# Performance work log

Hardware: AMD Instinct MI355X
Metric: run time of the kernel (lower is better)

## Reference

```python
import jax, jax.numpy as jnp
import numpy as np

FEATURE_DIM = 256


def setup_inputs() -> dict:
    key = jax.random.key(0)
    ks = jax.random.split(key, 8)
    B, C, H, W = 4, FEATURE_DIM, 64, 64
    s = 1.0 / np.sqrt(C)
    return {
        "x1": jax.random.normal(ks[0], (B, C, H, W), dtype=jnp.float32),
        "x2": jax.random.normal(ks[1], (B, C, H, W), dtype=jnp.float32),
        "Wq": jax.random.uniform(ks[2], (C, C), jnp.float32, -s, s),
        "bq": jax.random.uniform(ks[3], (C,), jnp.float32, -s, s),
        "Wk": jax.random.uniform(ks[4], (C, C), jnp.float32, -s, s),
        "bk": jax.random.uniform(ks[5], (C,), jnp.float32, -s, s),
        "Wv": jax.random.uniform(ks[6], (C, C), jnp.float32, -s, s),
        "bv": jax.random.uniform(ks[7], (C,), jnp.float32, -s, s),
    }


def _linear(x, W, b):
    # torch nn.Linear: x @ W.T + b
    return jnp.einsum("bnc,dc->bnd", x, W) + b


def reference(x1, x2, Wq, bq, Wk, bk, Wv, bv):
    B, C, H, W = x1.shape
    # flatten spatial -> tokens: [B, N, C]
    t1 = x1.reshape(B, C, H * W).transpose(0, 2, 1)
    t2 = x2.reshape(B, C, H * W).transpose(0, 2, 1)

    q1, k1, v1 = _linear(t1, Wq, bq), _linear(t1, Wk, bk), _linear(t1, Wv, bv)
    q2, k2, v2 = _linear(t2, Wq, bq), _linear(t2, Wk, bk), _linear(t2, Wv, bv)

    # NOTE: original module has NO 1/sqrt(d) scaling, and attends to v of the
    # SAME stream as the query (x1_out uses v1, x2_out uses v2) — keep faithful.
    a1 = jax.nn.softmax(jnp.einsum("bnc,bmc->bnm", q1, k2), axis=-1)
    a2 = jax.nn.softmax(jnp.einsum("bnc,bmc->bnm", q2, k1), axis=-1)

    o1 = jnp.einsum("bnm,bmc->bnc", a1, v1)
    o2 = jnp.einsum("bnm,bmc->bnc", a2, v2)

    x1_out = o1.transpose(0, 2, 1).reshape(B, C, H, W)
    x2_out = o2.transpose(0, 2, 1).reshape(B, C, H, W)
    return (x1_out, x2_out)
```

## Files before the change

### kernel.cpp

```cpp
#include <hip/hip_runtime.h>
#include <hip/hip_bf16.h>
#include <string.h>

typedef _Float16 half8 __attribute__((ext_vector_type(8)));
typedef _Float16 half4 __attribute__((ext_vector_type(4)));
typedef float f32x4 __attribute__((ext_vector_type(4)));
typedef float f32x16 __attribute__((ext_vector_type(16)));

#define NTOK 4096
#define CDIM 256

#define GLD_LDS16(g, l) __builtin_amdgcn_global_load_lds( \
    (const __attribute__((address_space(1))) void*)(g), \
    (__attribute__((address_space(3))) void*)(l), 16, 0, 0)

static __device__ __forceinline__ unsigned pk16(float a, float b) {
    auto h = __builtin_amdgcn_cvt_pkrtz(a, b);
    unsigned u;
    __builtin_memcpy(&u, &h, 4);
    return u;
}

__global__ __launch_bounds__(256, 2) void proj_kernel(
    const float* __restrict__ x1, const float* __restrict__ x2,
    const float* __restrict__ Wq, const float* __restrict__ bq,
    const float* __restrict__ Wk, const float* __restrict__ bk,
    const float* __restrict__ Wv, const float* __restrict__ bv,
    _Float16* __restrict__ Qh, _Float16* __restrict__ Kh,
    _Float16* __restrict__ Vt)
{
    __shared__ __align__(16) _Float16 Xl[64][264];
    __shared__ __align__(16) _Float16 Wl[64][264];
    __shared__ __align__(16) _Float16 Ol[64][68];

    const int t = threadIdx.x;
    const int lane = t & 63;
    const int w = t >> 6;
    const int bs = blockIdx.x >> 6;
    const int ntile = blockIdx.x & 63;
    const int n0 = ntile * 64;
    const int s = bs & 1, b = bs >> 1;

    const float* x = (s ? x2 : x1) + (size_t)b * CDIM * NTOK;

#pragma unroll
    for (int i = 0; i < 16; i++) {
        int id = t + 256 * i;
        int c = id >> 4, n4 = (id & 15) * 4;
        float4 v = *(const float4*)(x + (size_t)c * NTOK + n0 + n4);
        Xl[n4 + 0][c] = (_Float16)v.x;
        Xl[n4 + 1][c] = (_Float16)v.y;
        Xl[n4 + 2][c] = (_Float16)v.z;
        Xl[n4 + 3][c] = (_Float16)v.w;
    }

    for (int proj = 0; proj < 3; proj++) {
        const float* Wp = proj == 0 ? Wq : (proj == 1 ? Wk : Wv);
        const float* bp = proj == 0 ? bq : (proj == 1 ? bk : bv);
        for (int dt = 0; dt < 4; dt++) {
            const int d0 = dt * 64;
            __syncthreads();
#pragma unroll
            for (int i = 0; i < 16; i++) {
                int id = t + 256 * i;
                int d = id >> 6, c4 = (id & 63) * 4;
                float4 v = *(const float4*)(Wp + (size_t)(d0 + d) * CDIM + c4);
                half4 h = { (_Float16)v.x, (_Float16)v.y, (_Float16)v.z, (_Float16)v.w };
                *(half4*)&Wl[d][c4] = h;
            }
            __syncthreads();

            f32x4 acc[4];
            const f32x4 fz = {0.f, 0.f, 0.f, 0.f};
#pragma unroll
            for (int nt = 0; nt < 4; nt++) acc[nt] = fz;
#pragma unroll
            for (int cc = 0; cc < 8; cc++) {
                half8 wf = *(const half8*)&Wl[16 * w + (lane & 15)][cc * 32 + (lane >> 4) * 8];
#pragma unroll
                for (int nt = 0; nt < 4; nt++) {
                    half8 xf = *(const half8*)&Xl[nt * 16 + (lane & 15)][cc * 32 + (lane >> 4) * 8];
                    acc[nt] = __builtin_amdgcn_mfma_f32_16x16x32_f16(wf, xf, acc[nt], 0, 0, 0);
                }
            }
#pragma unroll
            for (int r = 0; r < 4; r++) {
                float bias = bp[d0 + 16 * w + (lane >> 4) * 4 + r];
#pragma unroll
                for (int nt = 0; nt < 4; nt++) {
                    _Float16 hv = (_Float16)(acc[nt][r] + bias);
                    if (proj < 2) Ol[nt * 16 + (lane & 15)][16 * w + (lane >> 4) * 4 + r] = hv;
                    else          Ol[16 * w + (lane >> 4) * 4 + r][nt * 16 + (lane & 15)] = hv;
                }
            }
            __syncthreads();
            _Float16* dst;
            size_t stride;
            if (proj == 0)      { dst = Qh + ((size_t)bs * NTOK + n0) * CDIM + d0; stride = CDIM; }
            else if (proj == 1) { dst = Kh + ((size_t)bs * NTOK + n0) * CDIM + d0; stride = CDIM; }
            else                { dst = Vt + ((size_t)bs * CDIM + d0) * NTOK + n0; stride = NTOK; }
#pragma unroll
            for (int i = 0; i < 4; i++) {
                int id = t + 256 * i;
                int row = id >> 4, c4 = (id & 15) * 4;
                *(half4*)(dst + (size_t)row * stride + c4) = *(const half4*)&Ol[row][c4];
            }
        }
    }
}

__global__ __launch_bounds__(512, 2) void flash_kernel(
    const _Float16* __restrict__ Qh, const _Float16* __restrict__ Kh,
    const _Float16* __restrict__ Vt, float* __restrict__ out)
{
    __shared__ __align__(16) char smem[131072];

    const int t = threadIdx.x, lane = t & 63;
    const int w = t >> 6;
    const int qg = w >> 1, mg = w & 1;
    const int l5 = lane & 31, hi = lane >> 5;
    const int bs = blockIdx.x & 7;
    const int qt = blockIdx.x >> 3;
    const int n0 = qt * 128;
    const int s = bs & 1, b = bs >> 1;

    half8 qf[16];
    {
        const _Float16* qp = Qh + ((size_t)bs * NTOK + n0 + qg * 32 + l5) * CDIM + hi * 8;
#pragma unroll
        for (int cc = 0; cc < 16; cc++) qf[cc] = *(const half8*)(qp + cc * 16);
    }

    const int bsK = b * 2 + (s ^ 1);
    const uint4* const Ksrc = (const uint4*)(Kh + (size_t)bsK * NTOK * CDIM);
    const uint4* const Vsrc = (const uint4*)(Vt + (size_t)bs * CDIM * NTOK);

    float m_run = -1e30f, l_run = 0.f;
    f32x16 Oacc[8];
    const f32x16 FZ16 = {0,0,0,0,0,0,0,0,0,0,0,0,0,0,0,0};
#pragma unroll
    for (int ct = 0; ct < 8; ct++) Oacc[ct] = FZ16;

    auto stage = [&](int buf, int kt) {
        const int m0 = kt * 64;
        char* base = smem + buf * 65536;
        if (w < 4) {
#pragma unroll
            for (int i = 0; i < 8; i++) {
                int instr = w * 8 + i;
                int cc = instr >> 1, mt = instr & 1;
                GLD_LDS16(Ksrc + (size_t)(m0 + mt * 32 + l5) * 32 + cc * 2 + hi,
                          base + (instr * 64) * 16 + (hi * 32 + l5) * 16);
            }
        } else {
#pragma unroll
            for (int i = 0; i < 8; i++) {
                int instr = (w - 4) * 8 + i;
                int kcg = instr >> 3, ct = instr & 7;
                GLD_LDS16(Vsrc + (size_t)(ct * 32 + l5) * 512 + (m0 >> 3) + kcg * 2 + hi,
                          base + 32768 + (instr * 64) * 16 + (hi * 32 + l5) * 16);
            }
        }
    };

    stage(0, 0);
    __syncthreads();

    for (int kt = 0; kt < 64; kt++) {
        const int cur = kt & 1;
        if (kt < 63) stage(cur ^ 1, kt + 1);
        const char* Kb = smem + cur * 65536;
        const char* Vbuf = Kb + 32768;

        f32x16 sf = FZ16;
#pragma unroll
        for (int cc = 0; cc < 16; cc++) {
            half8 kf = *(const half8*)(Kb + (cc * 2 + mg) * 1024 + hi * 512 + l5 * 16);
            sf = __builtin_amdgcn_mfma_f32_32x32x16_f16(kf, qf[cc], sf, 0, 0, 0);
        }

        float pm = sf[0];
#pragma unroll
        for (int r = 1; r < 16; r++) pm = fmaxf(pm, sf[r]);
        pm = fmaxf(pm, __shfl_xor(pm, 32));

        if (__any(pm > m_run + 8.0f)) {
            float nm = fmaxf(m_run, pm);
            float sc = __expf(m_run - nm);
            m_run = nm;
            l_run *= sc;
#pragma unroll
            for (int reg = 0; reg < 16; reg++) {
                float sr = __shfl(sc, (reg & 3) + 8 * (reg >> 2) + 4 * hi);
#pragma unroll
                for (int ct = 0; ct < 8; ct++) Oacc[ct][reg] *= sr;
            }
        }

        float lsum = 0.f;
#pragma unroll
        for (int r = 0; r < 16; r++) {
            float p = __expf(sf[r] - m_run);
            sf[r] = p;
            lsum += p;
        }
        lsum += __shfl_xor(lsum, 32);
        l_run += lsum;

        uint4 paw[2];
#pragma unroll
        for (int kc = 0; kc < 2; kc++) {
            const int qe = kc * 8;
            unsigned A01 = pk16(sf[qe + 0], sf[qe + 1]);
            unsigned A23 = pk16(sf[qe + 2], sf[qe + 3]);
            unsigned B01 = pk16(sf[qe + 4], sf[qe + 5]);
            unsigned B23 = pk16(sf[qe + 6], sf[qe + 7]);
            unsigned d0 = A01, s0 = B01;
            asm volatile("v_permlane32_swap_b32 %0, %1" : "+v"(d0), "+v"(s0));
            unsigned d1 = A23, s1 = B23;
            asm volatile("v_permlane32_swap_b32 %0, %1" : "+v"(d1), "+v"(s1));
            paw[kc].x = d0; paw[kc].y = d1; paw[kc].z = s0; paw[kc].w = s1;
        }

#pragma unroll
        for (int kc = 0; kc < 2; kc++) {
            half8 pa;
            __builtin_memcpy(&pa, &paw[kc], 16);
            const int kcg = mg * 2 + kc;
#pragma unroll
            for (int ct = 0; ct < 8; ct++) {
                half8 vf = *(const half8*)(Vbuf + ((kcg * 8 + ct) * 64) * 16
                                                 + (hi * 32 + l5) * 16);
                Oacc[ct] = __builtin_amdgcn_mfma_f32_32x32x16_f16(pa, vf, Oacc[ct], 0, 0, 0);
            }
        }

        __syncthreads();
    }

    float* const mlbuf = (float*)(smem + 65536);

    if (mg == 1 && hi == 0) {
        *(float2*)(mlbuf + (qg * 32 + l5) * 2) = make_float2(m_run, l_run);
    }
    if (mg == 1) {
#pragma unroll
        for (int ct = 0; ct < 4; ct++)
#pragma unroll
            for (int rc = 0; rc < 4; rc++) {
                f32x4 v = { Oacc[ct][rc*4+0], Oacc[ct][rc*4+1], Oacc[ct][rc*4+2], Oacc[ct][rc*4+3] };
                *(f32x4*)(smem + ((qg * 4 + ct) * 4 + rc) * 1024 + lane * 16) = v;
            }
    }
    __syncthreads();

    float a_s = 0.f, b_s = 0.f;
    if (mg == 0) {
        float2 ml = *(const float2*)(mlbuf + (qg * 32 + l5) * 2);
        float mstar = fmaxf(m_run, ml.x);
        float e0 = __expf(m_run - mstar), e1 = __expf(ml.x - mstar);
        float ltot = l_run * e0 + ml.y * e1;
        a_s = e0 / ltot; b_s = e1 / ltot;
#pragma unroll
        for (int ct = 0; ct < 4; ct++)
#pragma unroll
            for (int rc = 0; rc < 4; rc++) {
                f32x4 o1 = *(const f32x4*)(smem + ((qg * 4 + ct) * 4 + rc) * 1024 + lane * 16);
#pragma unroll
                for (int j = 0; j < 4; j++) {
                    int r = j + 8 * rc + 4 * hi;
                    Oacc[ct][rc*4+j] = Oacc[ct][rc*4+j] * __shfl(a_s, r) + o1[j] * __shfl(b_s, r);
                }
            }
    }
    __syncthreads();
    if (mg == 1) {
#pragma unroll
        for (int ct = 0; ct < 4; ct++)
#pragma unroll
            for (int rc = 0; rc < 4; rc++) {
                f32x4 v = { Oacc[ct+4][rc*4+0], Oacc[ct+4][rc*4+1], Oacc[ct+4][rc*4+2], Oacc[ct+4][rc*4+3] };
                *(f32x4*)(smem + ((qg * 4 + ct) * 4 + rc) * 1024 + lane * 16) = v;
            }
    }
    __syncthreads();
    if (mg == 0) {
#pragma unroll
        for (int ct = 0; ct < 4; ct++)
#pragma unroll
            for (int rc = 0; rc < 4; rc++) {
                f32x4 o1 = *(const f32x4*)(smem + ((qg * 4 + ct) * 4 + rc) * 1024 + lane * 16);
#pragma unroll
                for (int j = 0; j < 4; j++) {
                    int r = j + 8 * rc + 4 * hi;
                    Oacc[ct+4][rc*4+j] = Oacc[ct+4][rc*4+j] * __shfl(a_s, r) + o1[j] * __shfl(b_s, r);
                }
            }
    }

    float* obase = out + (size_t)(s * 4 + b) * CDIM * NTOK + n0;
    char* const Olp = smem;
#pragma unroll
    for (int h = 0; h < 2; h++) {
        __syncthreads();
        if (mg == 0) {
#pragma unroll
            for (int ct4 = 0; ct4 < 4; ct4++) {
                int ct = h * 4 + ct4;
                int cl = ct4 * 32 + l5;
#pragma unroll
                for (int reg = 0; reg < 16; reg++) {
                    int n = qg * 32 + (reg & 3) + 8 * (reg >> 2) + 4 * hi;
                    int byteoff = cl * 512 + n * 4;
                    *(float*)(Olp + (byteoff ^ ((cl & 7) << 4))) = Oacc[ct][reg];
                }
            }
        }
        __syncthreads();
#pragma unroll
        for (int i = 0; i < 8; i++) {
            int id = t + 512 * i;
            int c = id >> 5, nc = id & 31;
            f32x4 v = *(const f32x4*)(Olp + c * 512 + ((nc ^ (c & 7)) << 4));
            *(f32x4*)(obase + (size_t)(h * 128 + c) * NTOK + nc * 4) = v;
        }
    }
}

extern "C" void kernel_launch(void* const* d_in, const int* in_sizes, int n_in,
                              void* d_out, int out_size, void* d_ws, size_t ws_size,
                              hipStream_t stream) {
    const float* x1 = (const float*)d_in[0];
    const float* x2 = (const float*)d_in[1];
    const float* Wq = (const float*)d_in[2];
    const float* bq = (const float*)d_in[3];
    const float* Wk = (const float*)d_in[4];
    const float* bk = (const float*)d_in[5];
    const float* Wv = (const float*)d_in[6];
    const float* bv = (const float*)d_in[7];

    _Float16* Qh = (_Float16*)d_ws;
    _Float16* Kh = Qh + (size_t)8 * NTOK * CDIM;
    _Float16* Vt = Kh + (size_t)8 * NTOK * CDIM;

    proj_kernel<<<dim3(512), dim3(256), 0, stream>>>(x1, x2, Wq, bq, Wk, bk, Wv, bv, Qh, Kh, Vt);
    flash_kernel<<<dim3(256), dim3(512), 0, stream>>>(Qh, Kh, Vt, (float*)d_out);
}
```

Before: 308.0 us.

## Split attention over key halves with separate merge kernel and prescaled exp2 softmax

Adds a new path that pre-converts weights (folding log2e into Wq and bq) and inputs to fp16. It then runs projection from fp16 buffers and a 256-thread flash kernel that splits the key range into two halves across 512 blocks, writing fp16 partial outputs plus running max and sum. A merge kernel combines the two halves. This replaces the intra-block split-K reduction with a grid-level one and uses exp2 instead of expf. The cost is extra launches, an fp16 rounding of partial outputs, and extra global traffic for the partial results, and the path runs only when the workspace is large enough.

```diff
diff --git a/kernel.cpp b/kernel.cpp
--- a/kernel.cpp
+++ b/kernel.cpp
@@ -9,6 +9,7 @@
 
 #define NTOK 4096
 #define CDIM 256
+#define LOG2E 1.44269504f
 
 #define GLD_LDS16(g, l) __builtin_amdgcn_global_load_lds( \
     (const __attribute__((address_space(1))) void*)(g), \
@@ -19,6 +20,343 @@
     unsigned u;
     __builtin_memcpy(&u, &h, 4);
     return u;
+}
+
+
+__global__ __launch_bounds__(256) void cvtW_kernel(
+    const float* __restrict__ Wq, const float* __restrict__ Wk,
+    const float* __restrict__ Wv, _Float16* __restrict__ Wh)
+{
+    int pid = blockIdx.x * 256 + threadIdx.x;
+    int base = pid * 8;
+    int proj = base >> 16;
+    int within = base & 65535;
+    const float* src = (proj == 0 ? Wq : (proj == 1 ? Wk : Wv)) + within;
+    float sc = (proj == 0) ? LOG2E : 1.0f;
+    float4 a = *(const float4*)(src);
+    float4 b = *(const float4*)(src + 4);
+    half8 h = { (_Float16)(a.x*sc), (_Float16)(a.y*sc), (_Float16)(a.z*sc), (_Float16)(a.w*sc),
+                (_Float16)(b.x*sc), (_Float16)(b.y*sc), (_Float16)(b.z*sc), (_Float16)(b.w*sc) };
+    *(half8*)(Wh + base) = h;
+}
+
+__global__ __launch_bounds__(256) void cvtX_kernel(
+    const float* __restrict__ x1, const float* __restrict__ x2,
+    _Float16* __restrict__ Xt)
+{
+    __shared__ __align__(16) _Float16 Xl[64][264];
+    const int t = threadIdx.x;
+    const int bs = blockIdx.x >> 6;
+    const int n0 = (blockIdx.x & 63) * 64;
+    const int s = bs & 1, b = bs >> 1;
+    const float* x = (s ? x2 : x1) + (size_t)b * CDIM * NTOK;
+#pragma unroll
+    for (int i = 0; i < 16; i++) {
+        int id = t + 256 * i;
+        int c = id >> 4, n4 = (id & 15) * 4;
+        float4 v = *(const float4*)(x + (size_t)c * NTOK + n0 + n4);
+        Xl[n4 + 0][c] = (_Float16)v.x;
+        Xl[n4 + 1][c] = (_Float16)v.y;
+        Xl[n4 + 2][c] = (_Float16)v.z;
+        Xl[n4 + 3][c] = (_Float16)v.w;
+    }
+    __syncthreads();
+    uint4* dst = (uint4*)(Xt + ((size_t)bs * NTOK + n0) * CDIM);
+#pragma unroll
+    for (int i = 0; i < 8; i++) {
+        int id = t + 256 * i;
+        int row = id >> 5, ck = id & 31;
+        dst[(size_t)row * 32 + ck] = *(const uint4*)&Xl[row][ck * 8];
+    }
+}
+
+__global__ __launch_bounds__(256, 2) void proj2_kernel(
+    const _Float16* __restrict__ Xt, const _Float16* __restrict__ Wh,
+    const float* __restrict__ bq, const float* __restrict__ bk,
+    const float* __restrict__ bv,
+    _Float16* __restrict__ Qh, _Float16* __restrict__ Kh,
+    _Float16* __restrict__ Vt)
+{
+    __shared__ __align__(16) _Float16 Xl[64][264];
+    __shared__ __align__(16) _Float16 Wl[64][264];
+    __shared__ __align__(16) _Float16 Ol[64][68];
+
+    const int t = threadIdx.x;
+    const int lane = t & 63;
+    const int w = t >> 6;
+    const int bs = blockIdx.x >> 6;
+    const int n0 = (blockIdx.x & 63) * 64;
+
+    const uint4* xsrc = (const uint4*)(Xt + ((size_t)bs * NTOK + n0) * CDIM);
+#pragma unroll
+    for (int i = 0; i < 8; i++) {
+        int id = t + 256 * i;
+        int row = id >> 5, ck = id & 31;
+        *(uint4*)&Xl[row][ck * 8] = xsrc[(size_t)row * 32 + ck];
+    }
+
+    for (int proj = 0; proj < 3; proj++) {
+        const float* bp = proj == 0 ? bq : (proj == 1 ? bk : bv);
+        const float bscale = (proj == 0) ? LOG2E : 1.0f;
+        for (int dt = 0; dt < 4; dt++) {
+            const int d0 = dt * 64;
+            __syncthreads();
+            const uint4* wsrc = (const uint4*)(Wh + ((size_t)proj * 256 + d0) * CDIM);
+#pragma unroll
+            for (int i = 0; i < 8; i++) {
+                int id = t + 256 * i;
+                int row = id >> 5, ck = id & 31;
+                *(uint4*)&Wl[row][ck * 8] = wsrc[(size_t)row * 32 + ck];
+            }
+            __syncthreads();
+
+            f32x4 acc[4];
+            const f32x4 fz = {0.f, 0.f, 0.f, 0.f};
+#pragma unroll
+            for (int nt = 0; nt < 4; nt++) acc[nt] = fz;
+#pragma unroll
+            for (int cc = 0; cc < 8; cc++) {
+                half8 wf = *(const half8*)&Wl[16 * w + (lane & 15)][cc * 32 + (lane >> 4) * 8];
+#pragma unroll
+                for (int nt = 0; nt < 4; nt++) {
+                    half8 xf = *(const half8*)&Xl[nt * 16 + (lane & 15)][cc * 32 + (lane >> 4) * 8];
+                    acc[nt] = __builtin_amdgcn_mfma_f32_16x16x32_f16(wf, xf, acc[nt], 0, 0, 0);
+                }
+            }
+#pragma unroll
+            for (int r = 0; r < 4; r++) {
+                float bias = bp[d0 + 16 * w + (lane >> 4) * 4 + r] * bscale;
+#pragma unroll
+                for (int nt = 0; nt < 4; nt++) {
+                    _Float16 hv = (_Float16)(acc[nt][r] + bias);
+                    if (proj < 2) Ol[nt * 16 + (lane & 15)][16 * w + (lane >> 4) * 4 + r] = hv;
+                    else          Ol[16 * w + (lane >> 4) * 4 + r][nt * 16 + (lane & 15)] = hv;
+                }
+            }
+            __syncthreads();
+            _Float16* dst;
+            size_t stride;
+            if (proj == 0)      { dst = Qh + ((size_t)bs * NTOK + n0) * CDIM + d0; stride = CDIM; }
+            else if (proj == 1) { dst = Kh + ((size_t)bs * NTOK + n0) * CDIM + d0; stride = CDIM; }
+            else                { dst = Vt + ((size_t)bs * CDIM + d0) * NTOK + n0; stride = NTOK; }
+#pragma unroll
+            for (int i = 0; i < 4; i++) {
+                int id = t + 256 * i;
+                int row = id >> 4, c4 = (id & 15) * 4;
+                *(half4*)(dst + (size_t)row * stride + c4) = *(const half4*)&Ol[row][c4];
+            }
+        }
+    }
+}
+
+__global__ __launch_bounds__(256, 2) void flash_half(
+    const _Float16* __restrict__ Qh, const _Float16* __restrict__ Kh,
+    const _Float16* __restrict__ Vt, _Float16* __restrict__ Op,
+    float* __restrict__ Ml)
+{
+    __shared__ __align__(16) char smem[65536];
+
+    const int t = threadIdx.x, lane = t & 63;
+    const int w = t >> 6;
+    const int l5 = lane & 31, hi = lane >> 5;
+    const int bid = blockIdx.x;
+    const int bs = bid & 7;
+    const int rest = bid >> 3;
+    const int qt = rest & 31;
+    const int h = rest >> 5;
+    const int n0 = qt * 128;
+    const int s = bs & 1, b = bs >> 1;
+    const int tokbase = h * 2048;
+
+    half8 qf[16];
+    {
+        const _Float16* qp = Qh + ((size_t)bs * NTOK + n0 + w * 32 + l5) * CDIM + hi * 8;
+#pragma unroll
+        for (int cc = 0; cc < 16; cc++) qf[cc] = *(const half8*)(qp + cc * 16);
+    }
+
+    const int bsK = b * 2 + (s ^ 1);
+    const uint4* const Ku = (const uint4*)(Kh + (size_t)bsK * NTOK * CDIM);
+    const uint4* const Vu = (const uint4*)(Vt + (size_t)bs * CDIM * NTOK);
+
+    float m_run = -1e30f, l_run = 0.f;
+    f32x16 Oacc[8];
+    const f32x16 FZ16 = {0,0,0,0,0,0,0,0,0,0,0,0,0,0,0,0};
+#pragma unroll
+    for (int ct = 0; ct < 8; ct++) Oacc[ct] = FZ16;
+
+    auto stage = [&](int buf, int kt) {
+        const int m0 = tokbase + kt * 32;
+        char* base = smem + buf * 32768;
+#pragma unroll
+        for (int i = 0; i < 4; i++) {
+            int cc = w * 4 + i;
+            GLD_LDS16(Ku + (size_t)(m0 + l5) * 32 + cc * 2 + hi,
+                      base + cc * 1024 + lane * 16);
+        }
+#pragma unroll
+        for (int i = 0; i < 4; i++) {
+            int f = w * 4 + i;
+            int kc = f >> 3, ct = f & 7;
+            GLD_LDS16(Vu + (size_t)(ct * 32 + l5) * 512 + (m0 >> 3) + kc * 2 + hi,
+                      base + 16384 + f * 1024 + lane * 16);
+        }
+    };
+
+    stage(0, 0);
+    __syncthreads();
+
+    for (int kt = 0; kt < 64; kt++) {
+        const int cur = kt & 1;
+        if (kt < 63) stage(cur ^ 1, kt + 1);
+        const char* Kb = smem + cur * 32768;
+        const char* Vb = Kb + 16384;
+
+        f32x16 sfA = FZ16, sfB = FZ16;
+        __builtin_amdgcn_s_setprio(1);
+#pragma unroll
+        for (int cc = 0; cc < 8; cc++) {
+            half8 kfA = *(const half8*)(Kb + cc * 1024 + lane * 16);
+            half8 kfB = *(const half8*)(Kb + (cc + 8) * 1024 + lane * 16);
+            sfA = __builtin_amdgcn_mfma_f32_32x32x16_f16(kfA, qf[cc], sfA, 0, 0, 0);
+            sfB = __builtin_amdgcn_mfma_f32_32x32x16_f16(kfB, qf[cc + 8], sfB, 0, 0, 0);
+        }
+        __builtin_amdgcn_s_setprio(0);
+        f32x16 sf = sfA + sfB;
+
+        float pm = fmaxf(fmaxf(fmaxf(sf[0], sf[1]), fmaxf(sf[2], sf[3])),
+                         fmaxf(fmaxf(sf[4], sf[5]), fmaxf(sf[6], sf[7])));
+        float pm2 = fmaxf(fmaxf(fmaxf(sf[8], sf[9]), fmaxf(sf[10], sf[11])),
+                          fmaxf(fmaxf(sf[12], sf[13]), fmaxf(sf[14], sf[15])));
+        pm = fmaxf(pm, pm2);
+        pm = fmaxf(pm, __shfl_xor(pm, 32));
+
+        if (__any(pm > m_run + 11.54f)) {
+            float nm = fmaxf(m_run, pm);
+            float sc = exp2f(m_run - nm);
+            m_run = nm;
+            l_run *= sc;
+#pragma unroll
+            for (int reg = 0; reg < 16; reg++) {
+                float sr = __shfl(sc, (reg & 3) + 8 * (reg >> 2) + 4 * hi);
+#pragma unroll
+                for (int ct = 0; ct < 8; ct++) Oacc[ct][reg] *= sr;
+            }
+        }
+
+#pragma unroll
+        for (int r = 0; r < 16; r++) sf[r] = exp2f(sf[r] - m_run);
+
+        uint4 paw[2];
+#pragma unroll
+        for (int kc = 0; kc < 2; kc++) {
+            const int qe = kc * 8;
+            unsigned A01 = pk16(sf[qe + 0], sf[qe + 1]);
+            unsigned A23 = pk16(sf[qe + 2], sf[qe + 3]);
+            unsigned B01 = pk16(sf[qe + 4], sf[qe + 5]);
+            unsigned B23 = pk16(sf[qe + 6], sf[qe + 7]);
+            unsigned d0 = A01, s0 = B01;
+            asm volatile("v_permlane32_swap_b32 %0, %1" : "+v"(d0), "+v"(s0));
+            unsigned d1 = A23, s1 = B23;
+            asm volatile("v_permlane32_swap_b32 %0, %1" : "+v"(d1), "+v"(s1));
+            paw[kc].x = d0; paw[kc].y = d1; paw[kc].z = s0; paw[kc].w = s1;
+        }
+
+        __builtin_amdgcn_s_setprio(1);
+#pragma unroll
+        for (int kc = 0; kc < 2; kc++) {
+            half8 pa;
+            __builtin_memcpy(&pa, &paw[kc], 16);
+#pragma unroll
+            for (int ct = 0; ct < 8; ct++) {
+                half8 vf = *(const half8*)(Vb + (kc * 8 + ct) * 1024 + lane * 16);
+                Oacc[ct] = __builtin_amdgcn_mfma_f32_32x32x16_f16(pa, vf, Oacc[ct], 0, 0, 0);
+            }
+        }
+        __builtin_amdgcn_s_setprio(0);
+
+        float lsum = ((sf[0] + sf[1]) + (sf[2] + sf[3])) + ((sf[4] + sf[5]) + (sf[6] + sf[7]))
+                   + ((sf[8] + sf[9]) + (sf[10] + sf[11])) + ((sf[12] + sf[13]) + (sf[14] + sf[15]));
+        lsum += __shfl_xor(lsum, 32);
+        l_run += lsum;
+
+        __syncthreads();
+    }
+
+    if (hi == 0) {
+        float2 ml = make_float2(m_run, l_run);
+        *(float2*)(Ml + ((size_t)(h * 8 + bs) * NTOK + n0 + w * 32 + l5) * 2) = ml;
+    }
+
+    _Float16* const Olp = (_Float16*)smem;
+#pragma unroll
+    for (int hcc = 0; hcc < 2; hcc++) {
+        __syncthreads();
+#pragma unroll
+        for (int ct4 = 0; ct4 < 4; ct4++) {
+            int ct = hcc * 4 + ct4;
+            int cl = ct4 * 32 + l5;
+#pragma unroll
+            for (int reg = 0; reg < 16; reg++) {
+                int n = w * 32 + (reg & 3) + 8 * (reg >> 2) + 4 * hi;
+                Olp[cl * 136 + n] = (_Float16)Oacc[ct][reg];
+            }
+        }
+        __syncthreads();
+        _Float16* obase = Op + ((size_t)(h * 8 + bs) * CDIM + hcc * 128) * NTOK + n0;
+#pragma unroll
+        for (int i = 0; i < 8; i++) {
+            int id = t + 256 * i;
+            int c = id >> 4, ch = id & 15;
+            *(uint4*)(obase + (size_t)c * NTOK + ch * 8) = *(const uint4*)&Olp[c * 136 + ch * 8];
+        }
+    }
+}
+
+__global__ __launch_bounds__(256) void merge_kernel(
+    const _Float16* __restrict__ Op, const float* __restrict__ Ml,
+    float* __restrict__ out)
+{
+    __shared__ float w0s[256], w1s[256];
+    const int t = threadIdx.x;
+    const int bid = blockIdx.x;
+    const int bs = bid & 7;
+    const int cb = (bid >> 3) & 7;
+    const int nb = bid >> 6;
+    const int s = bs & 1, b = bs >> 1;
+
+    {
+        int n = nb * 256 + t;
+        float2 ml0 = *(const float2*)(Ml + ((size_t)(0 + bs) * NTOK + n) * 2);
+        float2 ml1 = *(const float2*)(Ml + ((size_t)(8 + bs) * NTOK + n) * 2);
+        float mstar = fmaxf(ml0.x, ml1.x);
+        float e0 = exp2f(ml0.x - mstar), e1 = exp2f(ml1.x - mstar);
+        float inv = 1.0f / (e0 * ml0.y + e1 * ml1.y);
+        w0s[t] = e0 * inv;
+        w1s[t] = e1 * inv;
+    }
+    __syncthreads();
+
+    const size_t cbase0 = ((size_t)(0 + bs) * CDIM + cb * 32) * NTOK + nb * 256;
+    const size_t cbase1 = ((size_t)(8 + bs) * CDIM + cb * 32) * NTOK + nb * 256;
+    float* obase = out + ((size_t)(s * 4 + b) * CDIM + cb * 32) * NTOK + nb * 256;
+#pragma unroll
+    for (int i = 0; i < 4; i++) {
+        int id = t + 256 * i;
+        int c = id >> 5, nc = (id & 31) * 8;
+        half8 a = *(const half8*)(Op + cbase0 + (size_t)c * NTOK + nc);
+        half8 d = *(const half8*)(Op + cbase1 + (size_t)c * NTOK + nc);
+        float4 o0, o1;
+        float* op = &o0.x;
+#pragma unroll
+        for (int j = 0; j < 8; j++) {
+            float v = w0s[nc + j] * (float)a[j] + w1s[nc + j] * (float)d[j];
+            if (j < 4) (&o0.x)[j] = v; else (&o1.x)[j - 4] = v;
+        }
+        (void)op;
+        *(float4*)(obase + (size_t)c * NTOK + nc) = o0;
+        *(float4*)(obase + (size_t)c * NTOK + nc + 4) = o1;
+    }
 }
 
 __global__ __launch_bounds__(256, 2) void proj_kernel(
@@ -37,10 +375,8 @@
     const int lane = t & 63;
     const int w = t >> 6;
     const int bs = blockIdx.x >> 6;
-    const int ntile = blockIdx.x & 63;
-    const int n0 = ntile * 64;
+    const int n0 = (blockIdx.x & 63) * 64;
     const int s = bs & 1, b = bs >> 1;
-
     const float* x = (s ? x2 : x1) + (size_t)b * CDIM * NTOK;
 
 #pragma unroll
@@ -53,7 +389,6 @@
         Xl[n4 + 2][c] = (_Float16)v.z;
         Xl[n4 + 3][c] = (_Float16)v.w;
     }
-
     for (int proj = 0; proj < 3; proj++) {
         const float* Wp = proj == 0 ? Wq : (proj == 1 ? Wk : Wv);
         const float* bp = proj == 0 ? bq : (proj == 1 ? bk : bv);
@@ -65,11 +400,10 @@
                 int id = t + 256 * i;
                 int d = id >> 6, c4 = (id & 63) * 4;
                 float4 v = *(const float4*)(Wp + (size_t)(d0 + d) * CDIM + c4);
-                half4 h = { (_Float16)v.x, (_Float16)v.y, (_Float16)v.z, (_Float16)v.w };
-                *(half4*)&Wl[d][c4] = h;
+                half4 hh = { (_Float16)v.x, (_Float16)v.y, (_Float16)v.z, (_Float16)v.w };
+                *(half4*)&Wl[d][c4] = hh;
             }
             __syncthreads();
-
             f32x4 acc[4];
             const f32x4 fz = {0.f, 0.f, 0.f, 0.f};
 #pragma unroll
@@ -114,7 +448,6 @@
     const _Float16* __restrict__ Vt, float* __restrict__ out)
 {
     __shared__ __align__(16) char smem[131072];
-
     const int t = threadIdx.x, lane = t & 63;
     const int w = t >> 6;
     const int qg = w >> 1, mg = w & 1;
@@ -130,7 +463,6 @@
 #pragma unroll
         for (int cc = 0; cc < 16; cc++) qf[cc] = *(const half8*)(qp + cc * 16);
     }
-
     const int bsK = b * 2 + (s ^ 1);
     const uint4* const Ksrc = (const uint4*)(Kh + (size_t)bsK * NTOK * CDIM);
     const uint4* const Vsrc = (const uint4*)(Vt + (size_t)bs * CDIM * NTOK);
@@ -178,12 +510,10 @@
             half8 kf = *(const half8*)(Kb + (cc * 2 + mg) * 1024 + hi * 512 + l5 * 16);
             sf = __builtin_amdgcn_mfma_f32_32x32x16_f16(kf, qf[cc], sf, 0, 0, 0);
         }
-
         float pm = sf[0];
 #pragma unroll
         for (int r = 1; r < 16; r++) pm = fmaxf(pm, sf[r]);
         pm = fmaxf(pm, __shfl_xor(pm, 32));
-
         if (__any(pm > m_run + 8.0f)) {
             float nm = fmaxf(m_run, pm);
             float sc = __expf(m_run - nm);
@@ -196,7 +526,6 @@
                 for (int ct = 0; ct < 8; ct++) Oacc[ct][reg] *= sr;
             }
         }
-
         float lsum = 0.f;
 #pragma unroll
         for (int r = 0; r < 16; r++) {
@@ -221,7 +550,6 @@
             asm volatile("v_permlane32_swap_b32 %0, %1" : "+v"(d1), "+v"(s1));
             paw[kc].x = d0; paw[kc].y = d1; paw[kc].z = s0; paw[kc].w = s1;
         }
-
 #pragma unroll
         for (int kc = 0; kc < 2; kc++) {
             half8 pa;
@@ -229,17 +557,14 @@
             const int kcg = mg * 2 + kc;
 #pragma unroll
             for (int ct = 0; ct < 8; ct++) {
-                half8 vf = *(const half8*)(Vbuf + ((kcg * 8 + ct) * 64) * 16
-                                                 + (hi * 32 + l5) * 16);
+                half8 vf = *(const half8*)(Vbuf + ((kcg * 8 + ct) * 64) * 16 + (hi * 32 + l5) * 16);
                 Oacc[ct] = __builtin_amdgcn_mfma_f32_32x32x16_f16(pa, vf, Oacc[ct], 0, 0, 0);
             }
         }
-
         __syncthreads();
     }
 
     float* const mlbuf = (float*)(smem + 65536);
-
     if (mg == 1 && hi == 0) {
         *(float2*)(mlbuf + (qg * 32 + l5) * 2) = make_float2(m_run, l_run);
     }
@@ -253,7 +578,6 @@
             }
     }
     __syncthreads();
-
     float a_s = 0.f, b_s = 0.f;
     if (mg == 0) {
         float2 ml = *(const float2*)(mlbuf + (qg * 32 + l5) * 2);
@@ -297,16 +621,15 @@
                 }
             }
     }
-
     float* obase = out + (size_t)(s * 4 + b) * CDIM * NTOK + n0;
     char* const Olp = smem;
 #pragma unroll
-    for (int h = 0; h < 2; h++) {
+    for (int hh = 0; hh < 2; hh++) {
         __syncthreads();
         if (mg == 0) {
 #pragma unroll
             for (int ct4 = 0; ct4 < 4; ct4++) {
-                int ct = h * 4 + ct4;
+                int ct = hh * 4 + ct4;
                 int cl = ct4 * 32 + l5;
 #pragma unroll
                 for (int reg = 0; reg < 16; reg++) {
@@ -322,7 +645,7 @@
             int id = t + 512 * i;
             int c = id >> 5, nc = id & 31;
             f32x4 v = *(const f32x4*)(Olp + c * 512 + ((nc ^ (c & 7)) << 4));
-            *(f32x4*)(obase + (size_t)(h * 128 + c) * NTOK + nc * 4) = v;
+            *(f32x4*)(obase + (size_t)(hh * 128 + c) * NTOK + nc * 4) = v;
         }
     }
 }
@@ -339,10 +662,27 @@
     const float* Wv = (const float*)d_in[6];
     const float* bv = (const float*)d_in[7];
 
+    const size_t QKV_HALFS = (size_t)8 * NTOK * CDIM;
     _Float16* Qh = (_Float16*)d_ws;
-    _Float16* Kh = Qh + (size_t)8 * NTOK * CDIM;
-    _Float16* Vt = Kh + (size_t)8 * NTOK * CDIM;
-
-    proj_kernel<<<dim3(512), dim3(256), 0, stream>>>(x1, x2, Wq, bq, Wk, bk, Wv, bv, Qh, Kh, Vt);
-    flash_kernel<<<dim3(256), dim3(512), 0, stream>>>(Qh, Kh, Vt, (float*)d_out);
-}
+    _Float16* Kh = Qh + QKV_HALFS;
+    _Float16* Vt = Kh + QKV_HALFS;
+
+    const size_t NEED_A = 3 * QKV_HALFS * 2
+                        + 2 * QKV_HALFS * 2
+                        + (size_t)2 * 8 * NTOK * 2 * 4;
+
+    if (ws_size >= NEED_A) {
+        _Float16* Xt = Vt + QKV_HALFS;
+        _Float16* Op = Vt + QKV_HALFS;
+        float* Ml = (float*)(Op + 2 * QKV_HALFS);
+        _Float16* Wh = (_Float16*)(Ml + (size_t)2 * 8 * NTOK * 2);
+        cvtW_kernel<<<dim3(96), dim3(256), 0, stream>>>(Wq, Wk, Wv, Wh);
+        cvtX_kernel<<<dim3(512), dim3(256), 0, stream>>>(x1, x2, Xt);
+        proj2_kernel<<<dim3(512), dim3(256), 0, stream>>>(Xt, Wh, bq, bk, bv, Qh, Kh, Vt);
+        flash_half<<<dim3(512), dim3(256), 0, stream>>>(Qh, Kh, Vt, Op, Ml);
+        merge_kernel<<<dim3(1024), dim3(256), 0, stream>>>(Op, Ml, (float*)d_out);
+    } else {
+        proj_kernel<<<dim3(512), dim3(256), 0, stream>>>(x1, x2, Wq, bq, Wk, bk, Wv, bv, Qh, Kh, Vt);
+        flash_kernel<<<dim3(256), dim3(512), 0, stream>>>(Qh, Kh, Vt, (float*)d_out);
+    }
+}
```

Result: slower. 391.0 us (+26.9%).
